# Optimization experiments

Hardware: AMD Instinct MI355X
Metric: run time of the kernel (lower is better)

The kernel has to match this reference:

```python
import jax, jax.numpy as jnp
import numpy as np

OUTPUT_SIZE = (7, 7)
SPATIAL_SCALE = 0.0625
B, C, H, W = 4, 256, 38, 38
N_ROIS = 512
IMG = int(W / SPATIAL_SCALE)  # 608


def setup_inputs() -> dict:
    key = jax.random.key(0)
    k_feat, k_bidx, k_xy = jax.random.split(key, 3)
    features = jax.random.normal(k_feat, (B, C, H, W), dtype=jnp.float32)
    batch_idx = jax.random.randint(k_bidx, (N_ROIS, 1), 0, B).astype(jnp.float32)
    # (x1,x2) and (y1,y2) sampled in image coords, sorted so x1<=x2, y1<=y2
    xy = jax.random.uniform(k_xy, (N_ROIS, 2, 2), minval=0.0, maxval=float(IMG))
    xy = jnp.sort(xy, axis=2)  # [N, {x,y}, {lo,hi}]
    rois = jnp.concatenate(
        [batch_idx, xy[:, 0, 0:1], xy[:, 1, 0:1], xy[:, 0, 1:2], xy[:, 1, 1:2]],
        axis=1,
    ).astype(jnp.float32)  # [N,5] = (b, x1, y1, x2, y2)
    return {"features": features, "rois": rois}


def _roi_pool(features, rois, output_size, spatial_scale):
    Ph, Pw = output_size
    Bf, Cf, Hf, Wf = features.shape
    bidx = rois[:, 0].astype(jnp.int32)
    # torch .long() truncates toward zero; coords are non-negative here
    coords = jnp.trunc(rois[:, 1:5] * spatial_scale).astype(jnp.int32)
    x1 = jnp.clip(coords[:, 0], 0, Wf - 1)
    y1 = jnp.clip(coords[:, 1], 0, Hf - 1)
    x2 = jnp.clip(coords[:, 2], 0, Wf - 1)
    y2 = jnp.clip(coords[:, 3], 0, Hf - 1)
    hh = y2 - y1 + 1  # region height (inclusive slice y1:y2+1)
    ww = x2 - x1 + 1
    feat = features[bidx]  # [N,C,H,W] per-ROI gathered feature map
    hs = jnp.arange(Hf)
    ws = jnp.arange(Wf)
    NEG = jnp.finfo(features.dtype).min
    # adaptive_max_pool2d bins: start = floor(p*size/P), end = ceil((p+1)*size/P)
    # 2D max over a rectangle = max over rows then max over cols.
    rows = []
    for p in range(Ph):
        s = y1 + (p * hh) // Ph
        e = y1 + ((p + 1) * hh + Ph - 1) // Ph  # ceil div
        m = (hs[None, :] >= s[:, None]) & (hs[None, :] < e[:, None])  # [N,H]
        rows.append(jnp.max(jnp.where(m[:, None, :, None], feat, NEG), axis=2))  # [N,C,W]
    ry = jnp.stack(rows, axis=2)  # [N,C,Ph,W]
    cols = []
    for q in range(Pw):
        s = x1 + (q * ww) // Pw
        e = x1 + ((q + 1) * ww + Pw - 1) // Pw
        m = (ws[None, :] >= s[:, None]) & (ws[None, :] < e[:, None])  # [N,W]
        cols.append(jnp.max(jnp.where(m[:, None, None, :], ry, NEG), axis=3))  # [N,C,Ph]
    return jnp.stack(cols, axis=3)  # [N,C,Ph,Pw]


def reference(features, rois):
    return _roi_pool(features, rois, OUTPUT_SIZE, SPATIAL_SCALE)
```

## Files before the change

### kernel.cpp

```cpp
#include <hip/hip_runtime.h>


#define NROIS 512
#define CCH   256
#define FH    38
#define FW    38
#define HW    (FH * FW)
#define SCALE 0.0625f
#define NEGF  (-3.402823466e+38f)

#define FEATT_BYTES ((size_t)4 * HW * CCH * sizeof(float))

__device__ __forceinline__ void roi_decode(
    const float* __restrict__ rr,
    int& bb, int& x1, int& y1, int& x2, int& y2, int& hh, int& ww)
{
    bb = (int)rr[0];
    x1 = (int)(rr[1] * SCALE);
    y1 = (int)(rr[2] * SCALE);
    x2 = (int)(rr[3] * SCALE);
    y2 = (int)(rr[4] * SCALE);
    x1 = min(max(x1, 0), FW - 1);
    y1 = min(max(y1, 0), FH - 1);
    x2 = min(max(x2, 0), FW - 1);
    y2 = min(max(y2, 0), FH - 1);
    hh = y2 - y1 + 1;
    ww = x2 - x1 + 1;
}

__global__ __launch_bounds__(256) void transpose_sort_kernel(
    const float* __restrict__ src, const float* __restrict__ rois,
    float* __restrict__ dst, int* __restrict__ perm)
{
    __shared__ float tile[4][257];

    const int b  = blockIdx.y;
    const int s0 = blockIdx.x * 4;
    const int t  = threadIdx.x;

    const float4 v = *(const float4*)(src + ((size_t)(b * CCH + t)) * HW + s0);
    tile[0][t] = v.x; tile[1][t] = v.y; tile[2][t] = v.z; tile[3][t] = v.w;
    __syncthreads();

    const int s = t >> 6;
    const int m = t & 63;
    float* drow = dst + ((size_t)b * HW + s0 + s) * CCH;
    #pragma unroll
    for (int k = 0; k < 4; ++k)
        drow[m + 64 * k] = tile[s][m + 64 * k];

    if (blockIdx.x == 0 && blockIdx.y == 0) {
        __shared__ int hist[256];
        __shared__ int sc[256];

        hist[t] = 0;
        __syncthreads();

        int bb, x1, y1, x2, y2, hh, ww;
        roi_decode(rois + t * 5, bb, x1, y1, x2, y2, hh, ww);
        const int k0 = ((1444 - hh * ww) * 255) / 1443;
        roi_decode(rois + (t + 256) * 5, bb, x1, y1, x2, y2, hh, ww);
        const int k1 = ((1444 - hh * ww) * 255) / 1443;

        atomicAdd(&hist[k0], 1);
        atomicAdd(&hist[k1], 1);
        __syncthreads();

        const int own = hist[t];
        sc[t] = own;
        __syncthreads();
        #pragma unroll
        for (int off = 1; off < 256; off <<= 1) {
            const int u = (t >= off) ? sc[t - off] : 0;
            __syncthreads();
            sc[t] += u;
            __syncthreads();
        }
        hist[t] = sc[t] - own;
        __syncthreads();

        perm[atomicAdd(&hist[k0], 1)] = t;
        perm[atomicAdd(&hist[k1], 1)] = t + 256;
    }
}

template <int WW>
__device__ __forceinline__ void pool_one(
    const float* __restrict__ rb, int h, float (&acc)[7])
{
    for (int y = 0; y < h; ++y) {
        float v[WW];
        #pragma unroll
        for (int j = 0; j < WW; ++j) v[j] = rb[j * CCH];
        #pragma unroll
        for (int q = 0; q < 7; ++q) {
            const int xs = (q * WW) / 7;
            const int xe = ((q + 1) * WW + 6) / 7;
            #pragma unroll
            for (int j = xs; j < xe; ++j)
                acc[q] = fmaxf(acc[q], v[j]);
        }
        rb += (size_t)FW * CCH;
    }
}

__global__ __launch_bounds__(256) void roipool_kernel(
    const float* __restrict__ featT,
    const float* __restrict__ rois,
    const int* __restrict__ perm,
    float* __restrict__ out)
{
    __shared__ float smem[49][65];

    const int bid  = blockIdx.x;
    const int tid  = threadIdx.x;
    const int wv   = __builtin_amdgcn_readfirstlane(tid >> 6);
    const int lane = tid & 63;

    #pragma unroll 1
    for (int sit = 0; sit < 2; ++sit) {
        const int item = sit ? (2047 - bid) : bid;
        const int r  = perm[item >> 2];
        const int cg = item & 3;

        int bb, x1, y1, x2, y2, hh, ww;
        roi_decode(rois + r * 5, bb, x1, y1, x2, y2, hh, ww);

        const float* fb = featT + (size_t)bb * HW * CCH + cg * 64 + lane
                        + (size_t)x1 * CCH;

        for (int p = wv; p < 7; p += 4) {
            const int ys = y1 + (p * hh) / 7;
            const int h  = (y1 + ((p + 1) * hh + 6) / 7) - ys;

            const float* rb0 = fb + (size_t)(ys * FW) * CCH;

            float acc[7];
            #pragma unroll
            for (int q = 0; q < 7; ++q) acc[q] = NEGF;

            switch (ww) {
                case  1: pool_one< 1>(rb0, h, acc); break;
                case  2: pool_one< 2>(rb0, h, acc); break;
                case  3: pool_one< 3>(rb0, h, acc); break;
                case  4: pool_one< 4>(rb0, h, acc); break;
                case  5: pool_one< 5>(rb0, h, acc); break;
                case  6: pool_one< 6>(rb0, h, acc); break;
                case  7: pool_one< 7>(rb0, h, acc); break;
                case  8: pool_one< 8>(rb0, h, acc); break;
                case  9: pool_one< 9>(rb0, h, acc); break;
                case 10: pool_one<10>(rb0, h, acc); break;
                case 11: pool_one<11>(rb0, h, acc); break;
                case 12: pool_one<12>(rb0, h, acc); break;
                case 13: pool_one<13>(rb0, h, acc); break;
                case 14: pool_one<14>(rb0, h, acc); break;
                case 15: pool_one<15>(rb0, h, acc); break;
                case 16: pool_one<16>(rb0, h, acc); break;
                case 17: pool_one<17>(rb0, h, acc); break;
                case 18: pool_one<18>(rb0, h, acc); break;
                case 19: pool_one<19>(rb0, h, acc); break;
                case 20: pool_one<20>(rb0, h, acc); break;
                case 21: pool_one<21>(rb0, h, acc); break;
                case 22: pool_one<22>(rb0, h, acc); break;
                case 23: pool_one<23>(rb0, h, acc); break;
                case 24: pool_one<24>(rb0, h, acc); break;
                case 25: pool_one<25>(rb0, h, acc); break;
                case 26: pool_one<26>(rb0, h, acc); break;
                case 27: pool_one<27>(rb0, h, acc); break;
                case 28: pool_one<28>(rb0, h, acc); break;
                case 29: pool_one<29>(rb0, h, acc); break;
                case 30: pool_one<30>(rb0, h, acc); break;
                case 31: pool_one<31>(rb0, h, acc); break;
                case 32: pool_one<32>(rb0, h, acc); break;
                case 33: pool_one<33>(rb0, h, acc); break;
                case 34: pool_one<34>(rb0, h, acc); break;
                case 35: pool_one<35>(rb0, h, acc); break;
                case 36: pool_one<36>(rb0, h, acc); break;
                case 37: pool_one<37>(rb0, h, acc); break;
                default: pool_one<38>(rb0, h, acc); break;
            }

            #pragma unroll
            for (int q = 0; q < 7; ++q)
                smem[p * 7 + q][lane] = acc[q];
        }
        __syncthreads();

        float* outb = out + (size_t)r * (CCH * 49) + cg * (64 * 49);
        int flat = tid;
        int c  = tid / 49;
        int pq = tid - c * 49;
        #pragma unroll
        for (int k = 0; k < 13; ++k) {
            if (flat < 3136)
                outb[c * 49 + pq] = smem[pq][c];
            flat += 256;
            c += 5; pq += 11;
            if (pq >= 49) { pq -= 49; c += 1; }
        }
        __syncthreads();
    }
}

__global__ __launch_bounds__(256) void roipool_fallback(
    const float* __restrict__ feat,
    const float* __restrict__ rois,
    float* __restrict__ out)
{
    int idx = blockIdx.x * blockDim.x + threadIdx.x;
    int q = idx % 7;
    int t = idx / 7;
    int p = t % 7;
    t /= 7;
    int c = t % CCH;
    int n = t / CCH;

    int bb, x1, y1, x2, y2, hh, ww;
    roi_decode(rois + n * 5, bb, x1, y1, x2, y2, hh, ww);

    int ys = y1 + (p * hh) / 7, ye = y1 + ((p + 1) * hh + 6) / 7;
    int xs = x1 + (q * ww) / 7, xe = x1 + ((q + 1) * ww + 6) / 7;

    const float* base = feat + ((size_t)bb * CCH + c) * HW;
    float m = NEGF;
    for (int y = ys; y < ye; ++y)
        for (int x = xs; x < xe; ++x)
            m = fmaxf(m, base[y * FW + x]);
    out[idx] = m;
}

extern "C" void kernel_launch(void* const* d_in, const int* in_sizes, int n_in,
                              void* d_out, int out_size, void* d_ws, size_t ws_size,
                              hipStream_t stream) {
    const float* feat = (const float*)d_in[0];
    const float* rois = (const float*)d_in[1];
    float* out = (float*)d_out;

    const size_t need = FEATT_BYTES + NROIS * sizeof(int);
    if (ws_size < need) {
        const int total = NROIS * CCH * 49;
        roipool_fallback<<<(total + 255) / 256, 256, 0, stream>>>(feat, rois, out);
        return;
    }

    float* featT = (float*)d_ws;
    int*   perm  = (int*)((char*)d_ws + FEATT_BYTES);

    dim3 tg(HW / 4, 4);
    transpose_sort_kernel<<<tg, 256, 0, stream>>>(feat, rois, featT, perm);

    roipool_kernel<<<1024, 256, 0, stream>>>(featT, rois, perm, out);
}
```

Measured before the change: 26.99 us.

## Split ROI pooling work by row-half across blocks and use nontemporal output stores

Each block now handles four work items, one per channel group. For each item it takes a (ROI, row-half) slot, so every wave computes at most one output row and no wave loops over two rows. This replaces the old scheme of two items per block, each covering all seven rows. It aims to fix the imbalance where one wave did two rows while the others did one, and it shrinks shared memory. Output is written with nontemporal stores. In exchange, each half-item leaves one wave idle on the second half and adds more sync rounds.

```diff
diff --git a/kernel.cpp b/kernel.cpp
--- a/kernel.cpp
+++ b/kernel.cpp
@@ -104,13 +104,28 @@
     }
 }
 
+template <int NB>
+__device__ __forceinline__ void write_out(
+    float* __restrict__ outb, const float (*__restrict__ sm)[65], int tid)
+{
+    #pragma unroll
+    for (int flat = 0; flat < 64 * NB; flat += 256) {
+        const int f = flat + tid;
+        if (f < 64 * NB) {
+            const int c = f / NB;
+            const int l = f - c * NB;
+            __builtin_nontemporal_store(sm[l][c], &outb[c * 49 + l]);
+        }
+    }
+}
+
 __global__ __launch_bounds__(256) void roipool_kernel(
     const float* __restrict__ featT,
     const float* __restrict__ rois,
     const int* __restrict__ perm,
     float* __restrict__ out)
 {
-    __shared__ float smem[49][65];
+    __shared__ float smem[28][65];
 
     const int bid  = blockIdx.x;
     const int tid  = threadIdx.x;
@@ -118,22 +133,21 @@
     const int lane = tid & 63;
 
     #pragma unroll 1
-    for (int sit = 0; sit < 2; ++sit) {
-        const int item = sit ? (2047 - bid) : bid;
-        const int r  = perm[item >> 2];
-        const int cg = item & 3;
+    for (int cg = 0; cg < 4; ++cg) {
+        const int slot = (cg & 1) ? (1023 - bid) : bid;
+        const int r  = perm[slot >> 1];
+        const int ph = slot & 1;
 
         int bb, x1, y1, x2, y2, hh, ww;
         roi_decode(rois + r * 5, bb, x1, y1, x2, y2, hh, ww);
 
-        const float* fb = featT + (size_t)bb * HW * CCH + cg * 64 + lane
-                        + (size_t)x1 * CCH;
-
-        for (int p = wv; p < 7; p += 4) {
+        const int p = 4 * ph + wv;
+        if (p < 7) {
             const int ys = y1 + (p * hh) / 7;
             const int h  = (y1 + ((p + 1) * hh + 6) / 7) - ys;
 
-            const float* rb0 = fb + (size_t)(ys * FW) * CCH;
+            const float* rb0 = featT + (size_t)bb * HW * CCH + cg * 64 + lane
+                             + (size_t)(ys * FW + x1) * CCH;
 
             float acc[7];
             #pragma unroll
@@ -182,22 +196,13 @@
 
             #pragma unroll
             for (int q = 0; q < 7; ++q)
-                smem[p * 7 + q][lane] = acc[q];
-        }
-        __syncthreads();
-
-        float* outb = out + (size_t)r * (CCH * 49) + cg * (64 * 49);
-        int flat = tid;
-        int c  = tid / 49;
-        int pq = tid - c * 49;
-        #pragma unroll
-        for (int k = 0; k < 13; ++k) {
-            if (flat < 3136)
-                outb[c * 49 + pq] = smem[pq][c];
-            flat += 256;
-            c += 5; pq += 11;
-            if (pq >= 49) { pq -= 49; c += 1; }
-        }
+                smem[wv * 7 + q][lane] = acc[q];
+        }
+        __syncthreads();
+
+        float* outb = out + (size_t)r * (CCH * 49) + cg * (64 * 49) + ph * 28;
+        if (ph == 0) write_out<28>(outb, smem, tid);
+        else         write_out<21>(outb, smem, tid);
         __syncthreads();
     }
 }
```

After: 40.67 us. +50.6%, slower.

## Drop ROI area sort, use float2 channel loads with one ROI-half per block

Applied to the files above, without the earlier changes.

Removes the histogram/prefix-scan sort of ROIs by area and the paired big/small work scheduling. Each block now handles one ROI and a 128-channel half, with each lane loading float2 (two channels) per pixel. Output is written with nontemporal stores. This cuts the single serial sort block from the transpose kernel and widens the loads, but it loses the area-based load balancing and uses more registers per thread.

```diff
diff --git a/kernel.cpp b/kernel.cpp
--- a/kernel.cpp
+++ b/kernel.cpp
@@ -28,12 +28,10 @@
     ww = x2 - x1 + 1;
 }
 
-__global__ __launch_bounds__(256) void transpose_sort_kernel(
-    const float* __restrict__ src, const float* __restrict__ rois,
-    float* __restrict__ dst, int* __restrict__ perm)
+__global__ __launch_bounds__(256) void transpose_kernel(
+    const float* __restrict__ src, float* __restrict__ dst)
 {
     __shared__ float tile[4][257];
-
     const int b  = blockIdx.y;
     const int s0 = blockIdx.x * 4;
     const int t  = threadIdx.x;
@@ -48,57 +46,26 @@
     #pragma unroll
     for (int k = 0; k < 4; ++k)
         drow[m + 64 * k] = tile[s][m + 64 * k];
-
-    if (blockIdx.x == 0 && blockIdx.y == 0) {
-        __shared__ int hist[256];
-        __shared__ int sc[256];
-
-        hist[t] = 0;
-        __syncthreads();
-
-        int bb, x1, y1, x2, y2, hh, ww;
-        roi_decode(rois + t * 5, bb, x1, y1, x2, y2, hh, ww);
-        const int k0 = ((1444 - hh * ww) * 255) / 1443;
-        roi_decode(rois + (t + 256) * 5, bb, x1, y1, x2, y2, hh, ww);
-        const int k1 = ((1444 - hh * ww) * 255) / 1443;
-
-        atomicAdd(&hist[k0], 1);
-        atomicAdd(&hist[k1], 1);
-        __syncthreads();
-
-        const int own = hist[t];
-        sc[t] = own;
-        __syncthreads();
-        #pragma unroll
-        for (int off = 1; off < 256; off <<= 1) {
-            const int u = (t >= off) ? sc[t - off] : 0;
-            __syncthreads();
-            sc[t] += u;
-            __syncthreads();
-        }
-        hist[t] = sc[t] - own;
-        __syncthreads();
-
-        perm[atomicAdd(&hist[k0], 1)] = t;
-        perm[atomicAdd(&hist[k1], 1)] = t + 256;
-    }
 }
 
 template <int WW>
 __device__ __forceinline__ void pool_one(
-    const float* __restrict__ rb, int h, float (&acc)[7])
+    const float* __restrict__ rb, int h, float2 (&acc)[7])
 {
     for (int y = 0; y < h; ++y) {
-        float v[WW];
-        #pragma unroll
-        for (int j = 0; j < WW; ++j) v[j] = rb[j * CCH];
+        float2 v[WW];
+        #pragma unroll
+        for (int j = 0; j < WW; ++j)
+            v[j] = *(const float2*)(rb + j * CCH);
         #pragma unroll
         for (int q = 0; q < 7; ++q) {
             const int xs = (q * WW) / 7;
             const int xe = ((q + 1) * WW + 6) / 7;
             #pragma unroll
-            for (int j = xs; j < xe; ++j)
-                acc[q] = fmaxf(acc[q], v[j]);
+            for (int j = xs; j < xe; ++j) {
+                acc[q].x = fmaxf(acc[q].x, v[j].x);
+                acc[q].y = fmaxf(acc[q].y, v[j].y);
+            }
         }
         rb += (size_t)FW * CCH;
     }
@@ -107,98 +74,90 @@
 __global__ __launch_bounds__(256) void roipool_kernel(
     const float* __restrict__ featT,
     const float* __restrict__ rois,
-    const int* __restrict__ perm,
     float* __restrict__ out)
 {
-    __shared__ float smem[49][65];
-
-    const int bid  = blockIdx.x;
+    __shared__ float smem[49][130];
+
+    const int n    = blockIdx.y;
+    const int cg2  = blockIdx.x;
     const int tid  = threadIdx.x;
     const int wv   = __builtin_amdgcn_readfirstlane(tid >> 6);
     const int lane = tid & 63;
 
-    #pragma unroll 1
-    for (int sit = 0; sit < 2; ++sit) {
-        const int item = sit ? (2047 - bid) : bid;
-        const int r  = perm[item >> 2];
-        const int cg = item & 3;
-
-        int bb, x1, y1, x2, y2, hh, ww;
-        roi_decode(rois + r * 5, bb, x1, y1, x2, y2, hh, ww);
-
-        const float* fb = featT + (size_t)bb * HW * CCH + cg * 64 + lane
-                        + (size_t)x1 * CCH;
-
-        for (int p = wv; p < 7; p += 4) {
-            const int ys = y1 + (p * hh) / 7;
-            const int h  = (y1 + ((p + 1) * hh + 6) / 7) - ys;
-
-            const float* rb0 = fb + (size_t)(ys * FW) * CCH;
-
-            float acc[7];
-            #pragma unroll
-            for (int q = 0; q < 7; ++q) acc[q] = NEGF;
-
-            switch (ww) {
-                case  1: pool_one< 1>(rb0, h, acc); break;
-                case  2: pool_one< 2>(rb0, h, acc); break;
-                case  3: pool_one< 3>(rb0, h, acc); break;
-                case  4: pool_one< 4>(rb0, h, acc); break;
-                case  5: pool_one< 5>(rb0, h, acc); break;
-                case  6: pool_one< 6>(rb0, h, acc); break;
-                case  7: pool_one< 7>(rb0, h, acc); break;
-                case  8: pool_one< 8>(rb0, h, acc); break;
-                case  9: pool_one< 9>(rb0, h, acc); break;
-                case 10: pool_one<10>(rb0, h, acc); break;
-                case 11: pool_one<11>(rb0, h, acc); break;
-                case 12: pool_one<12>(rb0, h, acc); break;
-                case 13: pool_one<13>(rb0, h, acc); break;
-                case 14: pool_one<14>(rb0, h, acc); break;
-                case 15: pool_one<15>(rb0, h, acc); break;
-                case 16: pool_one<16>(rb0, h, acc); break;
-                case 17: pool_one<17>(rb0, h, acc); break;
-                case 18: pool_one<18>(rb0, h, acc); break;
-                case 19: pool_one<19>(rb0, h, acc); break;
-                case 20: pool_one<20>(rb0, h, acc); break;
-                case 21: pool_one<21>(rb0, h, acc); break;
-                case 22: pool_one<22>(rb0, h, acc); break;
-                case 23: pool_one<23>(rb0, h, acc); break;
-                case 24: pool_one<24>(rb0, h, acc); break;
-                case 25: pool_one<25>(rb0, h, acc); break;
-                case 26: pool_one<26>(rb0, h, acc); break;
-                case 27: pool_one<27>(rb0, h, acc); break;
-                case 28: pool_one<28>(rb0, h, acc); break;
-                case 29: pool_one<29>(rb0, h, acc); break;
-                case 30: pool_one<30>(rb0, h, acc); break;
-                case 31: pool_one<31>(rb0, h, acc); break;
-                case 32: pool_one<32>(rb0, h, acc); break;
-                case 33: pool_one<33>(rb0, h, acc); break;
-                case 34: pool_one<34>(rb0, h, acc); break;
-                case 35: pool_one<35>(rb0, h, acc); break;
-                case 36: pool_one<36>(rb0, h, acc); break;
-                case 37: pool_one<37>(rb0, h, acc); break;
-                default: pool_one<38>(rb0, h, acc); break;
-            }
-
-            #pragma unroll
-            for (int q = 0; q < 7; ++q)
-                smem[p * 7 + q][lane] = acc[q];
-        }
-        __syncthreads();
-
-        float* outb = out + (size_t)r * (CCH * 49) + cg * (64 * 49);
-        int flat = tid;
-        int c  = tid / 49;
-        int pq = tid - c * 49;
-        #pragma unroll
-        for (int k = 0; k < 13; ++k) {
-            if (flat < 3136)
-                outb[c * 49 + pq] = smem[pq][c];
-            flat += 256;
-            c += 5; pq += 11;
-            if (pq >= 49) { pq -= 49; c += 1; }
-        }
-        __syncthreads();
+    int bb, x1, y1, x2, y2, hh, ww;
+    roi_decode(rois + n * 5, bb, x1, y1, x2, y2, hh, ww);
+
+    const float* fb = featT + (size_t)bb * HW * CCH + cg2 * 128 + 2 * lane
+                    + (size_t)x1 * CCH;
+
+    for (int p = wv; p < 7; p += 4) {
+        const int ys = y1 + (p * hh) / 7;
+        const int h  = (y1 + ((p + 1) * hh + 6) / 7) - ys;
+
+        const float* rb0 = fb + (size_t)(ys * FW) * CCH;
+
+        float2 acc[7];
+        #pragma unroll
+        for (int q = 0; q < 7; ++q) { acc[q].x = NEGF; acc[q].y = NEGF; }
+
+        switch (ww) {
+            case  1: pool_one< 1>(rb0, h, acc); break;
+            case  2: pool_one< 2>(rb0, h, acc); break;
+            case  3: pool_one< 3>(rb0, h, acc); break;
+            case  4: pool_one< 4>(rb0, h, acc); break;
+            case  5: pool_one< 5>(rb0, h, acc); break;
+            case  6: pool_one< 6>(rb0, h, acc); break;
+            case  7: pool_one< 7>(rb0, h, acc); break;
+            case  8: pool_one< 8>(rb0, h, acc); break;
+            case  9: pool_one< 9>(rb0, h, acc); break;
+            case 10: pool_one<10>(rb0, h, acc); break;
+            case 11: pool_one<11>(rb0, h, acc); break;
+            case 12: pool_one<12>(rb0, h, acc); break;
+            case 13: pool_one<13>(rb0, h, acc); break;
+            case 14: pool_one<14>(rb0, h, acc); break;
+            case 15: pool_one<15>(rb0, h, acc); break;
+            case 16: pool_one<16>(rb0, h, acc); break;
+            case 17: pool_one<17>(rb0, h, acc); break;
+            case 18: pool_one<18>(rb0, h, acc); break;
+            case 19: pool_one<19>(rb0, h, acc); break;
+            case 20: pool_one<20>(rb0, h, acc); break;
+            case 21: pool_one<21>(rb0, h, acc); break;
+            case 22: pool_one<22>(rb0, h, acc); break;
+            case 23: pool_one<23>(rb0, h, acc); break;
+            case 24: pool_one<24>(rb0, h, acc); break;
+            case 25: pool_one<25>(rb0, h, acc); break;
+            case 26: pool_one<26>(rb0, h, acc); break;
+            case 27: pool_one<27>(rb0, h, acc); break;
+            case 28: pool_one<28>(rb0, h, acc); break;
+            case 29: pool_one<29>(rb0, h, acc); break;
+            case 30: pool_one<30>(rb0, h, acc); break;
+            case 31: pool_one<31>(rb0, h, acc); break;
+            case 32: pool_one<32>(rb0, h, acc); break;
+            case 33: pool_one<33>(rb0, h, acc); break;
+            case 34: pool_one<34>(rb0, h, acc); break;
+            case 35: pool_one<35>(rb0, h, acc); break;
+            case 36: pool_one<36>(rb0, h, acc); break;
+            case 37: pool_one<37>(rb0, h, acc); break;
+            default: pool_one<38>(rb0, h, acc); break;
+        }
+
+        #pragma unroll
+        for (int q = 0; q < 7; ++q) {
+            smem[p * 7 + q][2 * lane]     = acc[q].x;
+            smem[p * 7 + q][2 * lane + 1] = acc[q].y;
+        }
+    }
+    __syncthreads();
+
+    float* outb = out + (size_t)n * (CCH * 49) + cg2 * (128 * 49);
+    #pragma unroll
+    for (int k = 0; k < 25; ++k) {
+        const int f = k * 256 + tid;
+        if (f < 6272) {
+            const int c  = f / 49;
+            const int pq = f - c * 49;
+            __builtin_nontemporal_store(smem[pq][c], &outb[f]);
+        }
     }
 }
 
@@ -236,18 +195,17 @@
     const float* rois = (const float*)d_in[1];
     float* out = (float*)d_out;
 
-    const size_t need = FEATT_BYTES + NROIS * sizeof(int);
-    if (ws_size < need) {
+    if (ws_size < FEATT_BYTES) {
         const int total = NROIS * CCH * 49;
         roipool_fallback<<<(total + 255) / 256, 256, 0, stream>>>(feat, rois, out);
         return;
     }
 
     float* featT = (float*)d_ws;
-    int*   perm  = (int*)((char*)d_ws + FEATT_BYTES);
 
     dim3 tg(HW / 4, 4);
-    transpose_sort_kernel<<<tg, 256, 0, stream>>>(feat, rois, featT, perm);
-
-    roipool_kernel<<<1024, 256, 0, stream>>>(featT, rois, perm, out);
-}
+    transpose_kernel<<<tg, 256, 0, stream>>>(feat, featT);
+
+    dim3 pg(2, NROIS);
+    roipool_kernel<<<pg, 256, 0, stream>>>(featT, rois, out);
+}
```

Result: slower. 35.45 us (+31.3%).
